# Optimization experiments

Measured on AMD Instinct MI355X. Metric: run time of the kernel, lower is better.

The kernel has to match this reference:

```python
import jax, jax.numpy as jnp
import numpy as np

B, L, D_MODEL = 2, 2048, 256
D_STATE, D_CONV, EXPAND, HEADDIM = 128, 4, 4, 64
D_INNER = EXPAND * D_MODEL            # 1024
NHEADS = D_INNER // HEADDIM           # 16
CONV_DIM = D_INNER + 2 * D_STATE      # 1280
D_IN_PROJ = 2 * D_INNER + 2 * D_STATE + NHEADS  # 2320
CHUNK = 256
GN_EPS = float(np.finfo(np.float32).eps)
RMS_EPS = 1e-5


def _silu(x):
    return x * jax.nn.sigmoid(x)


def _segsum(x):
    # x: (..., T) -> (..., T, T); out[i, j] = sum_{j<k<=i} x[k] for i>=j else -inf
    T = x.shape[-1]
    cs = jnp.cumsum(x, -1)
    d = cs[..., :, None] - cs[..., None, :]
    mask = jnp.tril(jnp.ones((T, T), bool))
    return jnp.where(mask, d, -jnp.inf)


def _ssd(X, A, Bm, Cm):
    # Chunked SSD (Mamba2 ssd_minimal_discrete). X:(b,l,h,p) already dt-scaled,
    # A:(b,l,h) = dt * (-exp(A_log)), Bm/Cm:(b,l,n) with ngroups=1.
    b, l, h, p = X.shape
    c = l // CHUNK
    Xc = X.reshape(b, c, CHUNK, h, p)
    Ac = jnp.transpose(A.reshape(b, c, CHUNK, h), (0, 3, 1, 2))  # (b,h,c,Q)
    Bc = Bm.reshape(b, c, CHUNK, -1)
    Cc = Cm.reshape(b, c, CHUNK, -1)
    A_cs = jnp.cumsum(Ac, -1)                                    # (b,h,c,Q)
    Lmat = jnp.exp(_segsum(Ac))                                  # (b,h,c,Q,Q)
    CB = jnp.einsum('bcln,bcsn->bcls', Cc, Bc)                   # (b,c,Q,Q)
    Y_diag = jnp.einsum('bhcls,bcshp->bclhp', Lmat * CB[:, None], Xc)
    decay_states = jnp.exp(A_cs[..., -1:] - A_cs)                # (b,h,c,Q)
    states = jnp.einsum('bcln,bhcl,bclhp->bchpn', Bc, decay_states, Xc)
    states = jnp.concatenate([jnp.zeros_like(states[:, :1]), states], 1)  # (b,c+1,h,p,n)
    decay_chunk = jnp.exp(_segsum(jnp.pad(A_cs[..., -1], ((0, 0), (0, 0), (1, 0)))))  # (b,h,c+1,c+1)
    new_states = jnp.einsum('bhzc,bchpn->bzhpn', decay_chunk, states)[:, :-1]
    state_decay = jnp.exp(A_cs)                                  # (b,h,c,Q)
    Y_off = jnp.einsum('bcln,bchpn,bhcl->bclhp', Cc, new_states, state_decay)
    return (Y_diag + Y_off).reshape(b, l, h, p)


def _mamba2(u, in_w, conv_w, conv_b, dt_bias, A_log, Dh, norm_w, out_w):
    # u: (b, l, d_model)
    b, l, _ = u.shape
    zxbcdt = u @ in_w.T                                          # (b,l,D_IN_PROJ)
    z = zxbcdt[..., :D_INNER]
    xBC = zxbcdt[..., D_INNER:D_INNER + CONV_DIM]
    dt = jax.nn.softplus(zxbcdt[..., -NHEADS:] + dt_bias)        # (b,l,h)
    # causal depthwise conv over time
    xc = jnp.transpose(xBC, (0, 2, 1))                           # (b,C,l)
    xc = jax.lax.conv_general_dilated(xc, conv_w, (1,), [(D_CONV - 1, 0)],
                                      dimension_numbers=('NCH', 'OIH', 'NCH'),
                                      feature_group_count=CONV_DIM)
    xBC = _silu(jnp.transpose(xc + conv_b[None, :, None], (0, 2, 1)))
    x = xBC[..., :D_INNER].reshape(b, l, NHEADS, HEADDIM)
    Bm = xBC[..., D_INNER:D_INNER + D_STATE]
    Cm = xBC[..., D_INNER + D_STATE:]
    A = dt * (-jnp.exp(A_log))                                   # (b,l,h)
    y = _ssd(dt[..., None] * x, A, Bm, Cm) + x * Dh[None, None, :, None]
    y = y.reshape(b, l, D_INNER) * _silu(z)                      # gated
    y = y * jax.lax.rsqrt(jnp.mean(y * y, -1, keepdims=True) + RMS_EPS) * norm_w
    return y @ out_w.T                                           # (b,l,d_model)


def _resmamba(x, gn_w, gn_b, fp, bp, proj_w, proj_b):
    # GroupNorm(1, C) over (C, L) per sample
    mu = jnp.mean(x, (1, 2), keepdims=True)
    var = jnp.mean((x - mu) ** 2, (1, 2), keepdims=True)
    xn = (x - mu) * jax.lax.rsqrt(var + GN_EPS) * gn_w[None, :, None] + gn_b[None, :, None]
    t = jnp.transpose(xn, (0, 2, 1))                             # (B,L,C)
    fwd = _mamba2(t, *fp)
    bwd = jnp.flip(_mamba2(jnp.flip(t, 1), *bp), 1)
    r = jnp.concatenate([fwd + t, bwd + t], -1)                  # (B,L,2C)
    pr = r @ proj_w.T + proj_b                                   # (B,L,C)
    return x + jnp.transpose(pr, (0, 2, 1))


def setup_inputs():
    key = jax.random.key(0)
    ks = jax.random.split(key, 4)
    s = 0.02
    inp = {
        'x': jax.random.normal(ks[0], (B, D_MODEL, L), jnp.float32),
        'gn_w': jnp.ones((D_MODEL,), jnp.float32),
        'gn_b': jnp.zeros((D_MODEL,), jnp.float32),
        'proj_w': s * jax.random.normal(ks[1], (D_MODEL, 2 * D_MODEL), jnp.float32),
        'proj_b': jnp.zeros((D_MODEL,), jnp.float32),
    }
    for i, p in enumerate(('f', 'b')):
        kk = jax.random.split(ks[2 + i], 5)
        inp[p + '_in_w'] = s * jax.random.normal(kk[0], (D_IN_PROJ, D_MODEL), jnp.float32)
        inp[p + '_conv_w'] = s * jax.random.normal(kk[1], (CONV_DIM, 1, D_CONV), jnp.float32)
        inp[p + '_conv_b'] = jnp.zeros((CONV_DIM,), jnp.float32)
        inp[p + '_dt_bias'] = 0.1 * jax.random.normal(kk[2], (NHEADS,), jnp.float32)
        inp[p + '_A_log'] = jnp.log(jax.random.uniform(kk[3], (NHEADS,), jnp.float32, 1.0, 16.0))
        inp[p + '_D'] = jnp.ones((NHEADS,), jnp.float32)
        inp[p + '_norm_w'] = jnp.ones((D_INNER,), jnp.float32)
        inp[p + '_out_w'] = s * jax.random.normal(kk[4], (D_MODEL, D_INNER), jnp.float32)
    return inp


def reference(x, gn_w, gn_b, proj_w, proj_b,
              f_in_w, f_conv_w, f_conv_b, f_dt_bias, f_A_log, f_D, f_norm_w, f_out_w,
              b_in_w, b_conv_w, b_conv_b, b_dt_bias, b_A_log, b_D, b_norm_w, b_out_w):
    fp = (f_in_w, f_conv_w, f_conv_b, f_dt_bias, f_A_log, f_D, f_norm_w, f_out_w)
    bp = (b_in_w, b_conv_w, b_conv_b, b_dt_bias, b_A_log, b_D, b_norm_w, b_out_w)
    return _resmamba(x, gn_w, gn_b, fp, bp, proj_w, proj_b)
```

## Files before the change

kernel.cpp:

```cpp
#include <hip/hip_runtime.h>
#include <hip/hip_bf16.h>
#include <math.h>

using bf16 = __hip_bfloat16;

#define L_SEQ   2048
#define DMODEL  256
#define DINNER  1024
#define DSTATE  128
#define NH      16
#define HD      64
#define CONVDIM 1280
#define DPROJ   2320
#define NCHK    8
#define CT      256
#define BATCH   2
#define M_TOT   (BATCH*L_SEQ)

#define ACS_N   (BATCH*NH*NCHK*CT)
#define ST_N    ((size_t)BATCH*NCHK*NH*HD*DSTATE)
#define CB_N    ((size_t)BATCH*NCHK*CT*CT)

typedef __bf16 bf16x8_t __attribute__((ext_vector_type(8)));
typedef __bf16 bf16x4_t __attribute__((ext_vector_type(4)));
typedef float  f32x4_t  __attribute__((ext_vector_type(4)));

__device__ __forceinline__ float tof(bf16 v){ return __bfloat162float(v); }
__device__ __forceinline__ bf16  tob(float v){ return __float2bfloat16(v); }
__device__ __forceinline__ float expdec(float a){ return __expf(fminf(a, 0.f)); }

__global__ __launch_bounds__(256) void k_front(
    const float* __restrict__ iw0, const float* __restrict__ iw1, const float* __restrict__ pw,
    bf16* __restrict__ inw_bf, bf16* __restrict__ projw_bf,
    const float* __restrict__ ow0, const float* __restrict__ ow1,
    bf16* __restrict__ owt, bf16* __restrict__ psum,
    const float* __restrict__ x, float2* __restrict__ pbuf){
  __shared__ __bf16 tile[64][65];
  __shared__ float sh[8];
  int bz = blockIdx.x, t = threadIdx.x;
  if (bz < 1160){
    int dir = bz >= 580; int sub = dir ? bz - 580 : bz;
    const float* src = dir ? iw1 : iw0;
    bf16* dst = inw_bf + (size_t)dir*DPROJ*DMODEL;
    int i = (sub*256 + t)*4;
    float4 v = *(const float4*)(src + i);
    dst[i]   = tob(v.x); dst[i+1] = tob(v.y);
    dst[i+2] = tob(v.z); dst[i+3] = tob(v.w);
  } else if (bz < 1288){
    int i = ((bz-1160)*256 + t)*4;
    float4 v = *(const float4*)(pw + i);
    projw_bf[i]   = tob(v.x); projw_bf[i+1] = tob(v.y);
    projw_bf[i+2] = tob(v.z); projw_bf[i+3] = tob(v.w);
  } else if (bz < 1416){
    int sub = bz - 1288;
    int dir = sub >> 6; int tid = sub & 63;
    int k0 = (tid >> 2)*64, j0 = (tid & 3)*64;
    const float* src = dir ? ow1 : ow0;
    bf16* dst = owt + (size_t)dir*DINNER*DMODEL;
    #pragma unroll
    for (int it = 0; it < 2; ++it){
      int idx = t + it*256; int jj = idx >> 3; int k8 = (idx & 7)*8;
      float4 va = *(const float4*)&src[(size_t)(j0+jj)*DINNER + k0 + k8];
      float4 vb = *(const float4*)&src[(size_t)(j0+jj)*DINNER + k0 + k8 + 4];
      tile[k8+0][jj] = (__bf16)va.x; tile[k8+1][jj] = (__bf16)va.y;
      tile[k8+2][jj] = (__bf16)va.z; tile[k8+3][jj] = (__bf16)va.w;
      tile[k8+4][jj] = (__bf16)vb.x; tile[k8+5][jj] = (__bf16)vb.y;
      tile[k8+6][jj] = (__bf16)vb.z; tile[k8+7][jj] = (__bf16)vb.w;
    }
    __syncthreads();
    #pragma unroll
    for (int it = 0; it < 2; ++it){
      int idx = t + it*256; int kr = idx >> 3; int j8 = (idx & 7)*8;
      bf16x8_t o;
      #pragma unroll
      for (int i = 0; i < 8; ++i) o[i] = tile[kr][j8+i];
      *(bf16x8_t*)&dst[(size_t)(k0+kr)*DMODEL + j0 + j8] = o;
    }
  } else if (bz < 1448){
    int i = ((bz - 1416)*256 + t)*8;
    int j = i & 255;
    const float* row = pw + (size_t)(i >> 8)*(2*DMODEL);
    bf16x8_t o;
    #pragma unroll
    for (int c = 0; c < 8; ++c) o[c] = (__bf16)(row[j+c] + row[256+j+c]);
    *(bf16x8_t*)&psum[i] = o;
  } else {
    int sub = bz - 1448;
    int blk = sub & 127, b = sub >> 7;
    const float4* p = (const float4*)(x + (size_t)b*(DMODEL*L_SEQ) + (size_t)blk*4096);
    float s = 0.f, ss = 0.f;
    #pragma unroll
    for (int k = 0; k < 4; ++k){
      float4 v = p[t + k*256];
      s  += v.x + v.y + v.z + v.w;
      ss += v.x*v.x + v.y*v.y + v.z*v.z + v.w*v.w;
    }
    for (int o = 32; o > 0; o >>= 1){ s += __shfl_down(s, o, 64); ss += __shfl_down(ss, o, 64); }
    if ((t & 63) == 0){ sh[(t>>6)*2] = s; sh[(t>>6)*2+1] = ss; }
    __syncthreads();
    if (t == 0){
      s  = sh[0]+sh[2]+sh[4]+sh[6];
      ss = sh[1]+sh[3]+sh[5]+sh[7];
      pbuf[b*128 + blk] = make_float2(s, ss);
    }
  }
}

__global__ __launch_bounds__(256) void k_t(const float* __restrict__ x, const float* __restrict__ gw,
                                           const float* __restrict__ gb, const float2* __restrict__ pbuf,
                                           bf16* __restrict__ t_out){
  __shared__ float tile[64][65];
  __shared__ float sh[4];
  int l0 = blockIdx.x*64, c0 = blockIdx.y*64, b = blockIdx.z;
  int tid = threadIdx.x;
  float s = 0.f, ss = 0.f;
  if (tid < 128){ float2 v = pbuf[b*128 + tid]; s = v.x; ss = v.y; }
  for (int o = 32; o > 0; o >>= 1){ s += __shfl_down(s, o, 64); ss += __shfl_down(ss, o, 64); }
  if (tid < 128 && (tid & 63) == 0){ sh[(tid>>6)*2] = s; sh[(tid>>6)*2+1] = ss; }
  __syncthreads();
  float inv = 1.f/(float)(DMODEL*L_SEQ);
  float s0 = sh[0]+sh[2], ss0 = sh[1]+sh[3];
  float mu = s0*inv, var = ss0*inv - mu*mu;
  float istd = rsqrtf(fmaxf(var, 0.f) + 1.1920929e-07f);

  int lx = tid & 63, cy = tid >> 6;
  for (int cc = cy; cc < 64; cc += 4){
    float v = x[(size_t)b*DMODEL*L_SEQ + (size_t)(c0+cc)*L_SEQ + l0+lx];
    tile[cc][lx] = (v - mu)*istd;
  }
  __syncthreads();
  int cx = tid & 63, ly = tid >> 6;
  float w = gw[c0+cx], bb = gb[c0+cx];
  for (int ll = ly; ll < 64; ll += 4)
    t_out[((size_t)(b*L_SEQ) + l0+ll)*DMODEL + c0+cx] = tob(tile[cx][ll]*w + bb);
}

__global__ __launch_bounds__(256) void gemm_inproj(const bf16* __restrict__ A, const bf16* __restrict__ B,
                                                   bf16* __restrict__ z, bf16* __restrict__ xbc,
                                                   float* __restrict__ dtb,
                                                   const float* __restrict__ db0, const float* __restrict__ db1){
  __shared__ __align__(16) bf16 lds[2][(128+128)*40];
  const int lda = DMODEL, ldb = DMODEL, N = DPROJ;
  int dir = blockIdx.z;
  const bf16* Bd = B + (size_t)dir*(size_t)N*ldb;
  int orig = blockIdx.x;
  int swz = (orig & 7)*76 + (orig >> 3);
  int m0 = (swz & 31)*128;
  int n0 = (swz >> 5)*128;
  int t = threadIdx.x;
  int wave = t >> 6, lane = t & 63;
  int wm = (wave & 1)*64, wn = (wave >> 1)*64;
  int lrow = lane & 15, quad = lane >> 4, lk8 = quad*8;

  int r0 = t >> 2, o0 = (t & 3)*8;
  int r1 = r0 + 64;
  int am0 = m0 + r0, am1 = m0 + r1;
  if (dir){
    am0 = (am0 & ~(L_SEQ-1)) | ((L_SEQ-1) - (am0 & (L_SEQ-1)));
    am1 = (am1 & ~(L_SEQ-1)) | ((L_SEQ-1) - (am1 & (L_SEQ-1)));
  }
  int bn0 = n0 + r0; if (bn0 > N-1) bn0 = N-1;
  int bn1 = n0 + r1; if (bn1 > N-1) bn1 = N-1;
  const bf16* Ap0 = A + (size_t)am0*lda + o0;
  const bf16* Ap1 = A + (size_t)am1*lda + o0;
  const bf16* Bp0 = Bd + (size_t)bn0*ldb + o0;
  const bf16* Bp1 = Bd + (size_t)bn1*ldb + o0;

  f32x4_t acc[4][4];
  #pragma unroll
  for (int i = 0; i < 4; ++i)
    #pragma unroll
    for (int j = 0; j < 4; ++j) acc[i][j] = (f32x4_t){0,0,0,0};

  uint4 ua0 = *(const uint4*)Ap0,      ua1 = *(const uint4*)Ap1;
  uint4 ub0 = *(const uint4*)Bp0,      ub1 = *(const uint4*)Bp1;
  uint4 va0 = *(const uint4*)(Ap0+32), va1 = *(const uint4*)(Ap1+32);
  uint4 vb0 = *(const uint4*)(Bp0+32), vb1 = *(const uint4*)(Bp1+32);

#define STAGE(buf, A0_, A1_, B0_, B1_) \
  *(uint4*)&lds[buf][r0*40 + o0] = A0_; \
  *(uint4*)&lds[buf][r1*40 + o0] = A1_; \
  *(uint4*)&lds[buf][(128 + r0)*40 + o0] = B0_; \
  *(uint4*)&lds[buf][(128 + r1)*40 + o0] = B1_;

#define COMPUTE(buf) { \
  const bf16* cs = lds[buf]; \
  bf16x8_t bfr[4]; \
  _Pragma("unroll") \
  for (int ni = 0; ni < 4; ++ni) bfr[ni] = *(const bf16x8_t*)&cs[(128 + wn + ni*16 + lrow)*40 + lk8]; \
  _Pragma("unroll") \
  for (int mi = 0; mi < 4; ++mi){ \
    bf16x8_t af = *(const bf16x8_t*)&cs[(wm + mi*16 + lrow)*40 + lk8]; \
    _Pragma("unroll") \
    for (int ni = 0; ni < 4; ++ni) \
      acc[mi][ni] = __builtin_amdgcn_mfma_f32_16x16x32_bf16(af, bfr[ni], acc[mi][ni], 0, 0, 0); \
  } }

  STAGE(0, ua0, ua1, ub0, ub1)
  __syncthreads();
  for (int it = 0; it < 8; it += 2){
    if (it + 2 < 8){
      int kk = (it+2) << 5;
      ua0 = *(const uint4*)(Ap0+kk); ua1 = *(const uint4*)(Ap1+kk);
      ub0 = *(const uint4*)(Bp0+kk); ub1 = *(const uint4*)(Bp1+kk);
    }
    COMPUTE(0)
    STAGE(1, va0, va1, vb0, vb1)
    __syncthreads();
    if (it + 3 < 8){
      int kk = (it+3) << 5;
      va0 = *(const uint4*)(Ap0+kk); va1 = *(const uint4*)(Ap1+kk);
      vb0 = *(const uint4*)(Bp0+kk); vb1 = *(const uint4*)(Bp1+kk);
    }
    COMPUTE(1)
    if (it + 2 < 8){
      STAGE(0, ua0, ua1, ub0, ub1)
      __syncthreads();
    }
  }
#undef STAGE
#undef COMPUTE

  if (n0 < DINNER + CONVDIM){
    __syncthreads();
    __bf16* outs = (__bf16*)lds;
    #pragma unroll
    for (int mi = 0; mi < 4; ++mi)
      #pragma unroll
      for (int ni = 0; ni < 4; ++ni)
        #pragma unroll
        for (int r = 0; r < 4; ++r)
          outs[(wm + mi*16 + quad*4 + r)*132 + wn + ni*16 + lrow] = (__bf16)acc[mi][ni][r];
    __syncthreads();
    bf16* dst; int ldd, c0;
    if (n0 < DINNER){ dst = z   + (size_t)dir*M_TOT*DINNER;  ldd = DINNER;  c0 = n0; }
    else            { dst = xbc + (size_t)dir*M_TOT*CONVDIM; ldd = CONVDIM; c0 = n0 - DINNER; }
    #pragma unroll
    for (int itv = 0; itv < 8; ++itv){
      int v = t + itv*256;
      int row = v >> 4, cb = v & 15;
      *(bf16x8_t*)&dst[(size_t)(m0+row)*ldd + c0 + cb*8] =
          *(const bf16x8_t*)&outs[row*132 + cb*8];
    }
  } else {
    const float* db = dir ? db1 : db0;
    float* dtp = dtb + (size_t)dir*((size_t)M_TOT*NH);
    #pragma unroll
    for (int mi = 0; mi < 4; ++mi)
      #pragma unroll
      for (int ni = 0; ni < 4; ++ni)
        #pragma unroll
        for (int r = 0; r < 4; ++r){
          int m = m0 + wm + mi*16 + quad*4 + r;
          int n = n0 + wn + ni*16 + lrow;
          if (n < N){
            int h = n - (DINNER + CONVDIM);
            float xx = acc[mi][ni][r] + db[h];
            dtp[(size_t)m*NH + h] = (xx > 20.f) ? xx : log1pf(expf(xx));
          }
        }
  }
}

__global__ __launch_bounds__(256) void gemm_w(const bf16* __restrict__ P, const bf16* __restrict__ owt,
                                              bf16* __restrict__ W){
  __shared__ __align__(16) bf16 lds[2][(128+64)*40];
  int dir = blockIdx.z;
  int m0 = blockIdx.x*128, n0 = blockIdx.y*64;
  int t = threadIdx.x;
  int wave = t >> 6, lane = t & 63;
  int wm = (wave & 1)*64, wn = (wave >> 1)*32;
  int lrow = lane & 15, quad = lane >> 4, lk8 = quad*8;

  int r0 = t >> 2, o0 = (t & 3)*8;
  int r1 = r0 + 64;
  const bf16* Ap0 = P + (size_t)(m0 + r0)*(2*DMODEL) + dir*DMODEL + o0;
  const bf16* Ap1 = P + (size_t)(m0 + r1)*(2*DMODEL) + dir*DMODEL + o0;
  const bf16* Bp  = owt + (size_t)dir*DINNER*DMODEL + (size_t)(n0 + r0)*DMODEL + o0;

  f32x4_t acc[4][2];
  #pragma unroll
  for (int i = 0; i < 4; ++i){ acc[i][0] = (f32x4_t){0,0,0,0}; acc[i][1] = (f32x4_t){0,0,0,0}; }

  int nit = DMODEL >> 5;
  uint4 a0 = *(const uint4*)Ap0;
  uint4 a1 = *(const uint4*)Ap1;
  uint4 b0 = *(const uint4*)Bp;
  int st = 0;
  *(uint4*)&lds[0][r0*40 + o0] = a0;
  *(uint4*)&lds[0][r1*40 + o0] = a1;
  *(uint4*)&lds[0][(128 + r0)*40 + o0] = b0;
  __syncthreads();
  for (int it = 0; it < nit; ++it){
    bool more = (it+1 < nit);
    if (more){
      int kk = (it+1) << 5;
      a0 = *(const uint4*)(Ap0 + kk);
      a1 = *(const uint4*)(Ap1 + kk);
      b0 = *(const uint4*)(Bp + kk);
    }
    const bf16* cs = lds[st];
    bf16x8_t af[4], bfr[2];
    #pragma unroll
    for (int mi = 0; mi < 4; ++mi) af[mi] = *(const bf16x8_t*)&cs[(wm + mi*16 + lrow)*40 + lk8];
    #pragma unroll
    for (int ni = 0; ni < 2; ++ni) bfr[ni] = *(const bf16x8_t*)&cs[(128 + wn + ni*16 + lrow)*40 + lk8];
    #pragma unroll
    for (int mi = 0; mi < 4; ++mi)
      #pragma unroll
      for (int ni = 0; ni < 2; ++ni)
        acc[mi][ni] = __builtin_amdgcn_mfma_f32_16x16x32_bf16(af[mi], bfr[ni], acc[mi][ni], 0, 0, 0);
    if (more){
      st ^= 1;
      *(uint4*)&lds[st][r0*40 + o0] = a0;
      *(uint4*)&lds[st][r1*40 + o0] = a1;
      *(uint4*)&lds[st][(128 + r0)*40 + o0] = b0;
      __syncthreads();
    }
  }
  bf16* Wd = W + (size_t)dir*DMODEL*DINNER;
  #pragma unroll
  for (int mi = 0; mi < 4; ++mi)
    #pragma unroll
    for (int ni = 0; ni < 2; ++ni)
      #pragma unroll
      for (int r = 0; r < 4; ++r){
        int m = m0 + wm + mi*16 + quad*4 + r;
        int n = n0 + wn + ni*16 + lrow;
        Wd[(size_t)m*DINNER + n] = tob(acc[mi][ni][r]);
      }
}

__global__ __launch_bounds__(256) void gemm_final(const bf16* __restrict__ y, const bf16* __restrict__ tb,
                                                  const bf16* __restrict__ W, const bf16* __restrict__ psum,
                                                  const float* __restrict__ x, const float* __restrict__ pb,
                                                  float* __restrict__ out){
  __shared__ __align__(16) bf16 lds[2][(32+64)*40];
  __shared__ float tile[32][65];
  int orig = blockIdx.x;
  int swz = (orig & 7)*64 + (orig >> 3);
  int mt_ = swz & 127, nt_ = swz >> 7;
  int m0 = mt_*32, n0 = nt_*64;
  int t = threadIdx.x;
  int wave = t >> 6, lane = t & 63;
  int lrow = lane & 15, quad = lane >> 4, lk8 = quad*8;
  int wn = wave*16;

  f32x4_t acc[2];
  acc[0] = (f32x4_t){0,0,0,0}; acc[1] = (f32x4_t){0,0,0,0};

  int rA = t >> 2, oA = (t & 3)*8;

  #pragma unroll
  for (int ph = 0; ph < 3; ++ph){
    const bf16 *Ab, *Bb; int lda, ldb, K, rev;
    if (ph == 0){ Ab = y;                             lda = DINNER; K = DINNER; Bb = W;                             ldb = DINNER; rev = 0; }
    else if (ph == 1){ Ab = y + (size_t)M_TOT*DINNER; lda = DINNER; K = DINNER; Bb = W + (size_t)DMODEL*DINNER;     ldb = DINNER; rev = 1; }
    else { Ab = tb; lda = DMODEL; K = DMODEL; Bb = psum; ldb = DMODEL; rev = 0; }

    int am = m0 + rA;
    if (rev) am = (am & ~(L_SEQ-1)) | ((L_SEQ-1) - (am & (L_SEQ-1)));
    const bf16* Ap = Ab + (size_t)am*lda + oA;
    const bf16* Bp = Bb + (size_t)(n0 + rA)*ldb + oA;

    int nit = K >> 5;
    uint4 a0, b0;
    if (t < 128) a0 = *(const uint4*)Ap;
    b0 = *(const uint4*)Bp;
    __syncthreads();
    int st = 0;
    if (t < 128) *(uint4*)&lds[0][rA*40 + oA] = a0;
    *(uint4*)&lds[0][(32 + rA)*40 + oA] = b0;
    __syncthreads();
    for (int it = 0; it < nit; ++it){
      bool more = (it+1 < nit);
      if (more){
        int kk = (it+1) << 5;
        if (t < 128) a0 = *(const uint4*)(Ap + kk);
        b0 = *(const uint4*)(Bp + kk);
      }
      const bf16* cs = lds[st];
      bf16x8_t bq = *(const bf16x8_t*)&cs[(32 + wn + lrow)*40 + lk8];
      #pragma unroll
      for (int mt = 0; mt < 2; ++mt){
        bf16x8_t af = *(const bf16x8_t*)&cs[(mt*16 + lrow)*40 + lk8];
        acc[mt] = __builtin_amdgcn_mfma_f32_16x16x32_bf16(af, bq, acc[mt], 0, 0, 0);
      }
      if (more){
        st ^= 1;
        if (t < 128) *(uint4*)&lds[st][rA*40 + oA] = a0;
        *(uint4*)&lds[st][(32 + rA)*40 + oA] = b0;
        __syncthreads();
      }
    }
  }

  #pragma unroll
  for (int mt = 0; mt < 2; ++mt)
    #pragma unroll
    for (int r = 0; r < 4; ++r)
      tile[mt*16 + quad*4 + r][wn + lrow] = acc[mt][r];
  __syncthreads();
  int b = m0 >> 11, l0 = m0 & (L_SEQ-1);
  int tx = t & 31, ny = t >> 5;
  for (int nn = ny; nn < 64; nn += 8){
    int n = n0 + nn;
    size_t xi = (size_t)b*DMODEL*L_SEQ + (size_t)n*L_SEQ + l0 + tx;
    out[xi] = tile[tx][nn] + pb[n] + x[xi];
  }
}

__global__ __launch_bounds__(256) void k_conv(const bf16* __restrict__ xraw, const float* __restrict__ cw0,
                                              const float* __restrict__ cb0, const float* __restrict__ cw1,
                                              const float* __restrict__ cb1, bf16* __restrict__ xconv){
  int t = threadIdx.x;
  int tx = t & 31, ty = t >> 5;
  int ch0 = blockIdx.x*256 + tx*8;
  int z = blockIdx.z; int b = z & 1, dir = z >> 1;
  int lbase = blockIdx.y*32 + ty*4;
  const float* cw = dir ? cw1 : cw0;
  const float* cb = dir ? cb1 : cb0;
  const bf16* xr = xraw  + (size_t)dir*((size_t)M_TOT*CONVDIM) + (size_t)(b*L_SEQ)*CONVDIM + ch0;
  bf16* xcv      = xconv + (size_t)dir*((size_t)M_TOT*CONVDIM) + (size_t)(b*L_SEQ)*CONVDIM + ch0;

  float wk[4][8];
  #pragma unroll
  for (int c = 0; c < 8; ++c){
    float4 w = *(const float4*)&cw[(ch0+c)*4];
    wk[0][c] = w.x; wk[1][c] = w.y; wk[2][c] = w.z; wk[3][c] = w.w;
  }
  float bias[8];
  {
    float4 b0v = *(const float4*)&cb[ch0];
    float4 b1v = *(const float4*)&cb[ch0+4];
    bias[0]=b0v.x; bias[1]=b0v.y; bias[2]=b0v.z; bias[3]=b0v.w;
    bias[4]=b1v.x; bias[5]=b1v.y; bias[6]=b1v.z; bias[7]=b1v.w;
  }

  bf16x8_t zero;
  #pragma unroll
  for (int c = 0; c < 8; ++c) zero[c] = (__bf16)0.f;

  bf16x8_t win[4];
  #pragma unroll
  for (int k = 0; k < 3; ++k){
    int ls = lbase - 3 + k;
    win[k] = (ls >= 0) ? *(const bf16x8_t*)&xr[(size_t)ls*CONVDIM] : zero;
  }
  #pragma unroll
  for (int i = 0; i < 4; ++i){
    int l = lbase + i;
    win[3] = *(const bf16x8_t*)&xr[(size_t)l*CONVDIM];
    bf16x8_t outv;
    #pragma unroll
    for (int c = 0; c < 8; ++c){
      float a = bias[c] + (float)win[0][c]*wk[0][c] + (float)win[1][c]*wk[1][c]
                        + (float)win[2][c]*wk[2][c] + (float)win[3][c]*wk[3][c];
      outv[c] = (__bf16)(a / (1.f + __expf(-a)));
    }
    *(bf16x8_t*)&xcv[(size_t)l*CONVDIM] = outv;
    win[0] = win[1]; win[1] = win[2]; win[2] = win[3];
  }
}

__global__ __launch_bounds__(256) void k_states(const bf16* __restrict__ xconv, const float* __restrict__ dt,
                                                const float* __restrict__ Al0, const float* __restrict__ Al1,
                                                float* __restrict__ A_cs, float* __restrict__ states){
  int id0 = blockIdx.x;
  int dir = id0 >> 8; int id = id0 & 255;
  int h = id & 15; int bc = id >> 4; int ch = bc & 7; int b = bc >> 3;
  int t = threadIdx.x;
  __shared__ float s_acs[CT];
  __shared__ float w_s[CT];
  __shared__ __align__(16) __bf16 Xt[64*72];
  __shared__ __align__(16) __bf16 Bt[128*72];
  const bf16* xc = xconv + (size_t)dir*((size_t)M_TOT*CONVDIM);
  const float* dtp = dt + (size_t)dir*((size_t)M_TOT*NH);
  const float* Alog = dir ? Al1 : Al0;
  size_t rowbase = (size_t)(b*L_SEQ) + ch*CT;

  float dtv = dtp[(rowbase + t)*NH + h];
  s_acs[t] = -expf(Alog[h]) * dtv;
  __syncthreads();
  for (int off = 1; off < 256; off <<= 1){
    float v = (t >= off) ? s_acs[t-off] : 0.f;
    __syncthreads();
    s_acs[t] += v;
    __syncthreads();
  }
  A_cs[(size_t)dir*ACS_N + (size_t)((b*NH+h)*NCHK + ch)*CT + t] = s_acs[t];
  float alast = s_acs[CT-1];
  w_s[t] = dtv * __expf(fminf(alast - s_acs[t], 0.f));
  __syncthreads();

  int wave = t >> 6, lane = t & 63, lrow = lane & 15, quad = lane >> 4;
  f32x4_t acc[8];
  #pragma unroll
  for (int i = 0; i < 8; ++i) acc[i] = (f32x4_t){0.f,0.f,0.f,0.f};

  for (int kt = 0; kt < 4; ++kt){
    int l0 = kt*64;
    #pragma unroll
    for (int it = 0; it < 2; ++it){
      int idx = t + it*256; int l = idx >> 3; int p0 = (idx & 7)*8;
      bf16x8_t v = *(const bf16x8_t*)&xc[(rowbase + l0 + l)*CONVDIM + h*HD + p0];
      float w = w_s[l0 + l];
      int col = (((l>>3) ^ ((p0>>3)&7))<<3) | (l&7);
      #pragma unroll
      for (int j = 0; j < 8; ++j) Xt[(p0+j)*72 + col] = (__bf16)((float)v[j]*w);
    }
    #pragma unroll
    for (int it = 0; it < 4; ++it){
      int idx = t + it*256; int l = idx >> 4; int n0 = (idx & 15)*8;
      bf16x8_t v = *(const bf16x8_t*)&xc[(rowbase + l0 + l)*CONVDIM + DINNER + n0];
      int col = (((l>>3) ^ ((n0>>3)&7))<<3) | (l&7);
      #pragma unroll
      for (int j = 0; j < 8; ++j) Bt[(n0+j)*72 + col] = v[j];
    }
    __syncthreads();
    int arow = wave*16 + lrow;
    #pragma unroll
    for (int ks = 0; ks < 2; ++ks){
      int kg = ks*4 + quad;
      bf16x8_t af = *(const bf16x8_t*)&Xt[arow*72 + ((kg ^ ((arow>>3)&7))<<3)];
      #pragma unroll
      for (int nt = 0; nt < 8; ++nt){
        int brow = nt*16 + lrow;
        bf16x8_t bq = *(const bf16x8_t*)&Bt[brow*72 + ((kg ^ ((brow>>3)&7))<<3)];
        acc[nt] = __builtin_amdgcn_mfma_f32_16x16x32_bf16(af, bq, acc[nt], 0, 0, 0);
      }
    }
    __syncthreads();
  }
  float* so = states + (size_t)dir*ST_N + (size_t)id*HD*DSTATE;
  int m = wave*16 + quad*4;
  #pragma unroll
  for (int nt = 0; nt < 8; ++nt)
    #pragma unroll
    for (int r = 0; r < 4; ++r)
      so[(size_t)(m+r)*DSTATE + nt*16 + lrow] = acc[nt][r];
}

__global__ __launch_bounds__(256) void k_recur(float* __restrict__ states, const float* __restrict__ A_cs){
  int blk = blockIdx.x;
  int bh2 = blk >> 5;
  int e = (blk & 31)*256 + threadIdx.x;
  int dir = bh2 >> 5; int bh = bh2 & 31;
  int h = bh & 15, b = bh >> 4;
  const float* ac = A_cs + (size_t)dir*ACS_N;
  float* st = states + (size_t)dir*ST_N;
  float s = 0.f;
  #pragma unroll
  for (int ch = 0; ch < NCHK; ++ch){
    float dec = expdec(ac[((size_t)(bh*NCHK+ch))*CT + CT-1]);
    size_t off = (size_t)(((b*NCHK+ch)*NH)+h)*HD*DSTATE + e;
    float cur = st[off];
    st[off] = s;
    s = s*dec + cur;
  }
}

__global__ __launch_bounds__(256) void k_cb(const bf16* __restrict__ xconv, float* __restrict__ CB){
  int zz = blockIdx.z;
  int dir = zz >> 4; int b = (zz >> 3) & 1; int ch = zz & 7;
  int m0 = blockIdx.x*64, n0 = blockIdx.y*64;
  if (n0 > m0) return;
  const bf16* base = xconv + (size_t)dir*((size_t)M_TOT*CONVDIM) + (size_t)(b*L_SEQ + ch*CT)*CONVDIM;
  const bf16* Crow = base + DINNER + DSTATE;
  const bf16* Brow = base + DINNER;
  __shared__ __align__(16) __bf16 As[64*136];
  __shared__ __align__(16) __bf16 Bs[64*136];
  int t = threadIdx.x;
  int r = t >> 2, o0 = (t & 3)*32;
  #pragma unroll
  for (int j = 0; j < 4; ++j){
    *(bf16x8_t*)&As[r*136 + o0 + j*8] = *(const bf16x8_t*)&Crow[(size_t)(m0+r)*CONVDIM + o0 + j*8];
    *(bf16x8_t*)&Bs[r*136 + o0 + j*8] = *(const bf16x8_t*)&Brow[(size_t)(n0+r)*CONVDIM + o0 + j*8];
  }
  __syncthreads();
  int wave = t >> 6, lane = t & 63, lrow = lane & 15, quad = lane >> 4;
  int wm = wave*16;
  f32x4_t acc[4];
  #pragma unroll
  for (int i = 0; i < 4; ++i) acc[i] = (f32x4_t){0.f,0.f,0.f,0.f};
  #pragma unroll
  for (int ks = 0; ks < 4; ++ks){
    bf16x8_t af = *(const bf16x8_t*)&As[(wm+lrow)*136 + ks*32 + quad*8];
    #pragma unroll
    for (int nt = 0; nt < 4; ++nt){
      bf16x8_t bq = *(const bf16x8_t*)&Bs[(nt*16+lrow)*136 + ks*32 + quad*8];
      acc[nt] = __builtin_amdgcn_mfma_f32_16x16x32_bf16(af, bq, acc[nt], 0, 0, 0);
    }
  }
  float* outp = CB + (size_t)dir*CB_N + (size_t)(b*NCHK+ch)*CT*CT;
  #pragma unroll
  for (int nt = 0; nt < 4; ++nt)
    #pragma unroll
    for (int r2 = 0; r2 < 4; ++r2)
      outp[(size_t)(m0+wm+quad*4+r2)*CT + n0+nt*16+lrow] = acc[nt][r2];
}

__global__ __launch_bounds__(512) void k_y_mfma(const bf16* __restrict__ xconv, const float* __restrict__ dt,
                                                const float* __restrict__ A_cs, const float* __restrict__ CB,
                                                const float* __restrict__ ns, bf16* __restrict__ y){
  int id0 = blockIdx.x;
  int dir = id0 >> 8; int id = id0 & 255;
  int h = id & 15; int bc = id >> 4; int ch = bc & 7; int b = bc >> 3;
  int t = threadIdx.x;
  int lane = t & 63;
  int lrow = lane & 15, quad = lane >> 4;

  __shared__ __align__(16) bf16 Xs[64*264];
  __shared__ __align__(16) bf16 NSs[64*136];
  __shared__ float acs_s[CT];

  const bf16* xc = xconv + (size_t)dir*((size_t)M_TOT*CONVDIM);
  const float* dtp = dt + (size_t)dir*((size_t)M_TOT*NH);
  const float* acs = A_cs + (size_t)dir*ACS_N + (size_t)((b*NH+h)*NCHK + ch)*CT;
  const float* cbz = CB + (size_t)dir*CB_N + (size_t)(b*NCHK+ch)*CT*CT;
  const float* nsp = ns + (size_t)dir*ST_N + (size_t)(((b*NCHK+ch)*NH)+h)*HD*DSTATE;
  bf16* yp = y + (size_t)dir*((size_t)M_TOT*DINNER);
  size_t rowbase = (size_t)(b*L_SEQ + ch*CT);
  if (t < CT) acs_s[t] = acs[t];

  #pragma unroll
  for (int it = 0; it < 4; ++it){
    int idx = t + it*512;
    int s = idx >> 3, p0 = (idx & 7)*8;
    float dtv = dtp[(rowbase + s)*NH + h];
    bf16x8_t v = *(const bf16x8_t*)&xc[(rowbase + s)*CONVDIM + h*HD + p0];
    int col = ((((s>>3) ^ ((p0>>3)&7)))<<3) | (s&7);
    #pragma unroll
    for (int j = 0; j < 8; ++j)
      Xs[(p0+j)*264 + col] = tob((float)v[j] * dtv);
  }
  for (int it = 0; it < 4; ++it){
    int idx = t + it*512;
    int n4 = (idx & 31)*4, p = idx >> 5;
    float4 v = *(const float4*)(nsp + p*DSTATE + n4);
    bf16* w = &NSs[p*136 + n4];
    w[0] = tob(v.x); w[1] = tob(v.y); w[2] = tob(v.z); w[3] = tob(v.w);
  }
  __syncthreads();

  int wave = t >> 6;
  int row0 = wave*32;
  float al0 = acs_s[row0 + lrow];
  float al1 = acs_s[row0 + 16 + lrow];
  float acs_r0 = acs_s[row0];

  f32x4_t acc[2][4];
  #pragma unroll
  for (int i = 0; i < 2; ++i)
    #pragma unroll
    for (int j = 0; j < 4; ++j) acc[i][j] = (f32x4_t){0.f,0.f,0.f,0.f};

  int nst = (row0 + 32) >> 5;
  for (int st = 0; st < nst; ++st){
    int s0 = st*32;
    if (s0 + 31 < row0 && (acs_r0 - acs_s[s0+31]) < -30.f) continue;
    int sg = (s0 >> 3) + quad;
    bf16x8_t bq[4];
    #pragma unroll
    for (int nt = 0; nt < 4; ++nt){
      int brow = nt*16 + lrow;
      bq[nt] = *(const bf16x8_t*)&Xs[brow*264 + ((sg ^ ((brow>>3)&7))<<3)];
    }
    bf16x8_t af[2];
    #pragma unroll
    for (int mt = 0; mt < 2; ++mt){
      int l = row0 + mt*16 + lrow;
      float al = mt ? al1 : al0;
      const float* cbrow = cbz + (size_t)l*CT + s0 + quad*8;
      float4 c0 = *(const float4*)cbrow;
      float4 c1 = *(const float4*)(cbrow + 4);
      float cv[8] = {c0.x,c0.y,c0.z,c0.w,c1.x,c1.y,c1.z,c1.w};
      union { bf16x8_t v; __bf16 e[8]; } wa;
      #pragma unroll
      for (int j = 0; j < 8; ++j){
        int s = s0 + quad*8 + j;
        float w = (s <= l) ? __expf(fminf(al - acs_s[s], 0.f)) * cv[j] : 0.f;
        wa.e[j] = (__bf16)w;
      }
      af[mt] = wa.v;
    }
    #pragma unroll
    for (int mt = 0; mt < 2; ++mt)
      #pragma unroll
      for (int nt = 0; nt < 4; ++nt)
        acc[mt][nt] = __builtin_amdgcn_mfma_f32_16x16x32_bf16(af[mt], bq[nt], acc[mt][nt], 0, 0, 0);
  }

  float el0 = __expf(fminf(al0, 0.f));
  float el1 = __expf(fminf(al1, 0.f));
  #pragma unroll
  for (int kt = 0; kt < 4; ++kt){
    int n0 = kt*32;
    bf16x8_t bq[4];
    #pragma unroll
    for (int nt = 0; nt < 4; ++nt)
      bq[nt] = *(const bf16x8_t*)&NSs[(nt*16+lrow)*136 + n0 + quad*8];
    bf16x8_t af[2];
    #pragma unroll
    for (int mt = 0; mt < 2; ++mt){
      int l = row0 + mt*16 + lrow;
      float el = mt ? el1 : el0;
      union { bf16x8_t v; __bf16 e[8]; } cu;
      cu.v = *(const bf16x8_t*)&xc[(rowbase + l)*CONVDIM + DINNER + DSTATE + n0 + quad*8];
      union { bf16x8_t v; __bf16 e[8]; } wa;
      #pragma unroll
      for (int j = 0; j < 8; ++j) wa.e[j] = (__bf16)((float)cu.e[j] * el);
      af[mt] = wa.v;
    }
    #pragma unroll
    for (int mt = 0; mt < 2; ++mt)
      #pragma unroll
      for (int nt = 0; nt < 4; ++nt)
        acc[mt][nt] = __builtin_amdgcn_mfma_f32_16x16x32_bf16(af[mt], bq[nt], acc[mt][nt], 0, 0, 0);
  }

  #pragma unroll
  for (int mt = 0; mt < 2; ++mt)
    #pragma unroll
    for (int nt = 0; nt < 4; ++nt)
      #pragma unroll
      for (int rr = 0; rr < 4; ++rr){
        int l = row0 + mt*16 + quad*4 + rr;
        int p = nt*16 + lrow;
        yp[(rowbase + l)*DINNER + h*HD + p] = tob(acc[mt][nt][rr]);
      }
}

__global__ __launch_bounds__(256) void k_gaterms(const bf16* __restrict__ z, const float* __restrict__ nw0,
                                                 const float* __restrict__ nw1, const bf16* __restrict__ xconv,
                                                 const float* __restrict__ Dh0, const float* __restrict__ Dh1,
                                                 bf16* __restrict__ y){
  int m0 = blockIdx.x;
  int dir = m0 >> 12; int m = m0 & (M_TOT-1);
  int t = threadIdx.x;
  const float* nw = dir ? nw1 : nw0;
  const float* Dh = dir ? Dh1 : Dh0;
  int j0 = t*4;
  const bf16* zp = z + (size_t)dir*((size_t)M_TOT*DINNER) + (size_t)m*DINNER;
  const bf16* xc = xconv + (size_t)dir*((size_t)M_TOT*CONVDIM) + (size_t)m*CONVDIM;
  bf16* yp = y + (size_t)dir*((size_t)M_TOT*DINNER) + (size_t)m*DINNER;

  bf16x4_t zv = *(const bf16x4_t*)&zp[j0];
  bf16x4_t yv = *(const bf16x4_t*)&yp[j0];
  bf16x4_t xv = *(const bf16x4_t*)&xc[j0];
  float Dv = Dh[j0 >> 6];
  float v[4]; float ss = 0.f;
  #pragma unroll
  for (int c = 0; c < 4; ++c){
    float zf = (float)zv[c];
    float raw = (float)yv[c] + Dv*(float)xv[c];
    float g = raw * (zf / (1.f + __expf(-zf)));
    v[c] = g; ss += g*g;
  }
  for (int o = 32; o > 0; o >>= 1) ss += __shfl_down(ss, o, 64);
  __shared__ float sh[4];
  if ((t & 63) == 0) sh[t>>6] = ss;
  __syncthreads();
  ss = sh[0]+sh[1]+sh[2]+sh[3];
  float scale = rsqrtf(ss*(1.f/DINNER) + 1e-5f);
  float4 nwv = *(const float4*)&nw[j0];
  float nws[4] = {nwv.x, nwv.y, nwv.z, nwv.w};
  bf16x4_t o;
  #pragma unroll
  for (int c = 0; c < 4; ++c) o[c] = (__bf16)(v[c]*scale*nws[c]);
  *(bf16x4_t*)&yp[j0] = o;
}

extern "C" void kernel_launch(void* const* d_in, const int* in_sizes, int n_in,
                              void* d_out, int out_size, void* d_ws, size_t ws_size,
                              hipStream_t stream){
  (void)in_sizes; (void)n_in; (void)out_size; (void)ws_size;
  const float* x      = (const float*)d_in[0];
  const float* gn_w   = (const float*)d_in[1];
  const float* gn_b   = (const float*)d_in[2];
  const float* proj_w = (const float*)d_in[3];
  const float* proj_b = (const float*)d_in[4];
  float* out = (float*)d_out;

  char* wp = (char*)d_ws;
  auto alloc = [&](size_t bytes){ void* r = (void*)wp; wp += (bytes + 255) & ~(size_t)255; return r; };
  bf16*  t_buf  = (bf16*) alloc((size_t)M_TOT*DMODEL*2);
  bf16*  z_buf  = (bf16*) alloc((size_t)2*M_TOT*DINNER*2);
  bf16*  xraw   = (bf16*) alloc((size_t)2*M_TOT*CONVDIM*2);
  bf16*  xconv  = (bf16*) alloc((size_t)2*M_TOT*CONVDIM*2);
  float* dt_buf = (float*)alloc((size_t)2*M_TOT*NH*4);
  float* acs    = (float*)alloc((size_t)2*ACS_N*4);
  float* states = (float*)alloc((size_t)2*ST_N*4);
  float* cb     = (float*)alloc((size_t)2*CB_N*4);
  float2* pbuf  = (float2*)alloc(BATCH*128*sizeof(float2));
  bf16*  inw_bf   = (bf16*)alloc((size_t)2*DPROJ*DMODEL*2);
  bf16*  projw_bf = (bf16*)alloc((size_t)DMODEL*2*DMODEL*2);
  bf16*  owt      = (bf16*)alloc((size_t)2*DINNER*DMODEL*2);
  bf16*  wfb      = (bf16*)alloc((size_t)2*DMODEL*DINNER*2);
  bf16*  psum     = (bf16*)alloc((size_t)DMODEL*DMODEL*2);
  bf16*  y_buf    = xraw;

  k_front<<<1704, 256, 0, stream>>>(
      (const float*)d_in[5], (const float*)d_in[13], proj_w,
      inw_bf, projw_bf,
      (const float*)d_in[12], (const float*)d_in[20], owt, psum,
      x, pbuf);

  gemm_w<<<dim3(2, 16, 2), 256, 0, stream>>>(projw_bf, owt, wfb);

  k_t<<<dim3(32,4,2), 256, 0, stream>>>(x, gn_w, gn_b, pbuf, t_buf);

  gemm_inproj<<<dim3(608, 1, 2), 256, 0, stream>>>(
      t_buf, inw_bf, z_buf, xraw, dt_buf,
      (const float*)d_in[8], (const float*)d_in[16]);

  k_conv<<<dim3(5, L_SEQ/32, 2*BATCH), 256, 0, stream>>>(
      xraw, (const float*)d_in[6], (const float*)d_in[7],
            (const float*)d_in[14], (const float*)d_in[15], xconv);
  k_states<<<2*BATCH*NCHK*NH, 256, 0, stream>>>(
      xconv, dt_buf, (const float*)d_in[9], (const float*)d_in[17], acs, states);
  k_recur<<<2*BATCH*NH*32, 256, 0, stream>>>(states, acs);
  k_cb<<<dim3(4,4,2*BATCH*NCHK), 256, 0, stream>>>(xconv, cb);
  k_y_mfma<<<2*BATCH*NCHK*NH, 512, 0, stream>>>(xconv, dt_buf, acs, cb, states, y_buf);
  k_gaterms<<<2*M_TOT, 256, 0, stream>>>(
      z_buf, (const float*)d_in[11], (const float*)d_in[19], xconv,
      (const float*)d_in[10], (const float*)d_in[18], y_buf);

  gemm_final<<<512, 256, 0, stream>>>(y_buf, t_buf, wfb, psum, x, proj_b, out);
}
```

Baseline: 227.5 us.

## Store CB and chunk states in bf16; widen gemm_final K-tile to 64

k_recur now writes the propagated chunk states to a separate bf16 buffer, and k_cb stages its output through LDS to write bf16 CB with vectorized stores. k_y_mfma reads both as bf16, which halves the bytes it loads and removes its per-element float-to-bf16 conversion. gemm_final moves from a 32-wide K step to a 64-wide one, with all threads loading and an unrolled double-buffered prologue, so it needs fewer barriers per K. Rounding CB to bf16 before the decay weighting adds a little extra error.

```diff
diff --git a/kernel.cpp b/kernel.cpp
--- a/kernel.cpp
+++ b/kernel.cpp
@@ -335,7 +335,7 @@
                                                   const bf16* __restrict__ W, const bf16* __restrict__ psum,
                                                   const float* __restrict__ x, const float* __restrict__ pb,
                                                   float* __restrict__ out){
-  __shared__ __align__(16) bf16 lds[2][(32+64)*40];
+  __shared__ __align__(16) bf16 lds[2][(32+64)*72];
   __shared__ float tile[32][65];
   int orig = blockIdx.x;
   int swz = (orig & 7)*64 + (orig >> 3);
@@ -349,7 +349,9 @@
   f32x4_t acc[2];
   acc[0] = (f32x4_t){0,0,0,0}; acc[1] = (f32x4_t){0,0,0,0};
 
-  int rA = t >> 2, oA = (t & 3)*8;
+  int rowA = t >> 3, oA = (t & 7)*8;
+  int rowB0 = t >> 3, oB0 = (t & 7)*8;
+  int rowB1 = (t + 256) >> 3, oB1 = (t & 7)*8;
 
   #pragma unroll
   for (int ph = 0; ph < 3; ++ph){
@@ -358,41 +360,60 @@
     else if (ph == 1){ Ab = y + (size_t)M_TOT*DINNER; lda = DINNER; K = DINNER; Bb = W + (size_t)DMODEL*DINNER;     ldb = DINNER; rev = 1; }
     else { Ab = tb; lda = DMODEL; K = DMODEL; Bb = psum; ldb = DMODEL; rev = 0; }
 
-    int am = m0 + rA;
+    int am = m0 + rowA;
     if (rev) am = (am & ~(L_SEQ-1)) | ((L_SEQ-1) - (am & (L_SEQ-1)));
-    const bf16* Ap = Ab + (size_t)am*lda + oA;
-    const bf16* Bp = Bb + (size_t)(n0 + rA)*ldb + oA;
-
-    int nit = K >> 5;
-    uint4 a0, b0;
-    if (t < 128) a0 = *(const uint4*)Ap;
-    b0 = *(const uint4*)Bp;
-    __syncthreads();
-    int st = 0;
-    if (t < 128) *(uint4*)&lds[0][rA*40 + oA] = a0;
-    *(uint4*)&lds[0][(32 + rA)*40 + oA] = b0;
-    __syncthreads();
-    for (int it = 0; it < nit; ++it){
-      bool more = (it+1 < nit);
-      if (more){
-        int kk = (it+1) << 5;
-        if (t < 128) a0 = *(const uint4*)(Ap + kk);
-        b0 = *(const uint4*)(Bp + kk);
+    const bf16* Ap  = Ab + (size_t)am*lda + oA;
+    const bf16* Bp0 = Bb + (size_t)(n0 + rowB0)*ldb + oB0;
+    const bf16* Bp1 = Bb + (size_t)(n0 + rowB1)*ldb + oB1;
+
+    int nit = K >> 6;
+    uint4 au  = *(const uint4*)Ap;
+    uint4 bu0 = *(const uint4*)Bp0;
+    uint4 bu1 = *(const uint4*)Bp1;
+    uint4 av  = *(const uint4*)(Ap + 64);
+    uint4 bv0 = *(const uint4*)(Bp0 + 64);
+    uint4 bv1 = *(const uint4*)(Bp1 + 64);
+
+#define FSTAGE(buf, A_, B0_, B1_) \
+    *(uint4*)&lds[buf][rowA*72 + oA] = A_; \
+    *(uint4*)&lds[buf][(32 + rowB0)*72 + oB0] = B0_; \
+    *(uint4*)&lds[buf][(32 + rowB1)*72 + oB1] = B1_;
+
+#define FCOMP(buf) { \
+    const bf16* cs = lds[buf]; \
+    _Pragma("unroll") \
+    for (int ks = 0; ks < 2; ++ks){ \
+      bf16x8_t bq = *(const bf16x8_t*)&cs[(32 + wn + lrow)*72 + ks*32 + lk8]; \
+      _Pragma("unroll") \
+      for (int mt = 0; mt < 2; ++mt){ \
+        bf16x8_t af = *(const bf16x8_t*)&cs[(mt*16 + lrow)*72 + ks*32 + lk8]; \
+        acc[mt] = __builtin_amdgcn_mfma_f32_16x16x32_bf16(af, bq, acc[mt], 0, 0, 0); \
+      } \
+    } }
+
+    __syncthreads();
+    FSTAGE(0, au, bu0, bu1)
+    __syncthreads();
+    for (int it = 0; it < nit; it += 2){
+      if (it + 2 < nit){
+        int kk = (it+2) << 6;
+        au = *(const uint4*)(Ap+kk); bu0 = *(const uint4*)(Bp0+kk); bu1 = *(const uint4*)(Bp1+kk);
       }
-      const bf16* cs = lds[st];
-      bf16x8_t bq = *(const bf16x8_t*)&cs[(32 + wn + lrow)*40 + lk8];
-      #pragma unroll
-      for (int mt = 0; mt < 2; ++mt){
-        bf16x8_t af = *(const bf16x8_t*)&cs[(mt*16 + lrow)*40 + lk8];
-        acc[mt] = __builtin_amdgcn_mfma_f32_16x16x32_bf16(af, bq, acc[mt], 0, 0, 0);
+      FCOMP(0)
+      FSTAGE(1, av, bv0, bv1)
+      __syncthreads();
+      if (it + 3 < nit){
+        int kk = (it+3) << 6;
+        av = *(const uint4*)(Ap+kk); bv0 = *(const uint4*)(Bp0+kk); bv1 = *(const uint4*)(Bp1+kk);
       }
-      if (more){
-        st ^= 1;
-        if (t < 128) *(uint4*)&lds[st][rA*40 + oA] = a0;
-        *(uint4*)&lds[st][(32 + rA)*40 + oA] = b0;
+      FCOMP(1)
+      if (it + 2 < nit){
+        FSTAGE(0, au, bu0, bu1)
         __syncthreads();
       }
     }
+#undef FSTAGE
+#undef FCOMP
   }
 
   #pragma unroll
@@ -541,26 +562,28 @@
       so[(size_t)(m+r)*DSTATE + nt*16 + lrow] = acc[nt][r];
 }
 
-__global__ __launch_bounds__(256) void k_recur(float* __restrict__ states, const float* __restrict__ A_cs){
+__global__ __launch_bounds__(256) void k_recur(const float* __restrict__ states, bf16* __restrict__ nsb,
+                                               const float* __restrict__ A_cs){
   int blk = blockIdx.x;
   int bh2 = blk >> 5;
   int e = (blk & 31)*256 + threadIdx.x;
   int dir = bh2 >> 5; int bh = bh2 & 31;
   int h = bh & 15, b = bh >> 4;
   const float* ac = A_cs + (size_t)dir*ACS_N;
-  float* st = states + (size_t)dir*ST_N;
+  const float* st = states + (size_t)dir*ST_N;
+  bf16* nb = nsb + (size_t)dir*ST_N;
   float s = 0.f;
   #pragma unroll
   for (int ch = 0; ch < NCHK; ++ch){
     float dec = expdec(ac[((size_t)(bh*NCHK+ch))*CT + CT-1]);
     size_t off = (size_t)(((b*NCHK+ch)*NH)+h)*HD*DSTATE + e;
     float cur = st[off];
-    st[off] = s;
+    nb[off] = tob(s);
     s = s*dec + cur;
   }
 }
 
-__global__ __launch_bounds__(256) void k_cb(const bf16* __restrict__ xconv, float* __restrict__ CB){
+__global__ __launch_bounds__(256) void k_cb(const bf16* __restrict__ xconv, bf16* __restrict__ CB){
   int zz = blockIdx.z;
   int dir = zz >> 4; int b = (zz >> 3) & 1; int ch = zz & 7;
   int m0 = blockIdx.x*64, n0 = blockIdx.y*64;
@@ -592,17 +615,25 @@
       acc[nt] = __builtin_amdgcn_mfma_f32_16x16x32_bf16(af, bq, acc[nt], 0, 0, 0);
     }
   }
-  float* outp = CB + (size_t)dir*CB_N + (size_t)(b*NCHK+ch)*CT*CT;
+  __syncthreads();
   #pragma unroll
   for (int nt = 0; nt < 4; ++nt)
     #pragma unroll
     for (int r2 = 0; r2 < 4; ++r2)
-      outp[(size_t)(m0+wm+quad*4+r2)*CT + n0+nt*16+lrow] = acc[nt][r2];
+      As[(wm + quad*4 + r2)*72 + nt*16 + lrow] = (__bf16)acc[nt][r2];
+  __syncthreads();
+  bf16* outp = CB + (size_t)dir*CB_N + (size_t)(b*NCHK+ch)*CT*CT;
+  #pragma unroll
+  for (int p = 0; p < 2; ++p){
+    int idx = t + p*256;
+    int row = idx >> 3, c8 = (idx & 7)*8;
+    *(bf16x8_t*)&outp[(size_t)(m0+row)*CT + n0 + c8] = *(const bf16x8_t*)&As[row*72 + c8];
+  }
 }
 
 __global__ __launch_bounds__(512) void k_y_mfma(const bf16* __restrict__ xconv, const float* __restrict__ dt,
-                                                const float* __restrict__ A_cs, const float* __restrict__ CB,
-                                                const float* __restrict__ ns, bf16* __restrict__ y){
+                                                const float* __restrict__ A_cs, const bf16* __restrict__ CB,
+                                                const bf16* __restrict__ ns, bf16* __restrict__ y){
   int id0 = blockIdx.x;
   int dir = id0 >> 8; int id = id0 & 255;
   int h = id & 15; int bc = id >> 4; int ch = bc & 7; int b = bc >> 3;
@@ -617,8 +648,8 @@
   const bf16* xc = xconv + (size_t)dir*((size_t)M_TOT*CONVDIM);
   const float* dtp = dt + (size_t)dir*((size_t)M_TOT*NH);
   const float* acs = A_cs + (size_t)dir*ACS_N + (size_t)((b*NH+h)*NCHK + ch)*CT;
-  const float* cbz = CB + (size_t)dir*CB_N + (size_t)(b*NCHK+ch)*CT*CT;
-  const float* nsp = ns + (size_t)dir*ST_N + (size_t)(((b*NCHK+ch)*NH)+h)*HD*DSTATE;
+  const bf16* cbz = CB + (size_t)dir*CB_N + (size_t)(b*NCHK+ch)*CT*CT;
+  const bf16* nsp = ns + (size_t)dir*ST_N + (size_t)(((b*NCHK+ch)*NH)+h)*HD*DSTATE;
   bf16* yp = y + (size_t)dir*((size_t)M_TOT*DINNER);
   size_t rowbase = (size_t)(b*L_SEQ + ch*CT);
   if (t < CT) acs_s[t] = acs[t];
@@ -634,12 +665,11 @@
     for (int j = 0; j < 8; ++j)
       Xs[(p0+j)*264 + col] = tob((float)v[j] * dtv);
   }
-  for (int it = 0; it < 4; ++it){
+  #pragma unroll
+  for (int it = 0; it < 2; ++it){
     int idx = t + it*512;
-    int n4 = (idx & 31)*4, p = idx >> 5;
-    float4 v = *(const float4*)(nsp + p*DSTATE + n4);
-    bf16* w = &NSs[p*136 + n4];
-    w[0] = tob(v.x); w[1] = tob(v.y); w[2] = tob(v.z); w[3] = tob(v.w);
+    int p = idx >> 4, n8 = (idx & 15)*8;
+    *(bf16x8_t*)&NSs[p*136 + n8] = *(const bf16x8_t*)&nsp[(size_t)p*DSTATE + n8];
   }
   __syncthreads();
 
@@ -671,15 +701,12 @@
     for (int mt = 0; mt < 2; ++mt){
       int l = row0 + mt*16 + lrow;
       float al = mt ? al1 : al0;
-      const float* cbrow = cbz + (size_t)l*CT + s0 + quad*8;
-      float4 c0 = *(const float4*)cbrow;
-      float4 c1 = *(const float4*)(cbrow + 4);
-      float cv[8] = {c0.x,c0.y,c0.z,c0.w,c1.x,c1.y,c1.z,c1.w};
+      bf16x8_t cvv = *(const bf16x8_t*)&cbz[(size_t)l*CT + s0 + quad*8];
       union { bf16x8_t v; __bf16 e[8]; } wa;
       #pragma unroll
       for (int j = 0; j < 8; ++j){
         int s = s0 + quad*8 + j;
-        float w = (s <= l) ? __expf(fminf(al - acs_s[s], 0.f)) * cv[j] : 0.f;
+        float w = (s <= l) ? __expf(fminf(al - acs_s[s], 0.f)) * (float)cvv[j] : 0.f;
         wa.e[j] = (__bf16)w;
       }
       af[mt] = wa.v;
@@ -791,7 +818,8 @@
   float* dt_buf = (float*)alloc((size_t)2*M_TOT*NH*4);
   float* acs    = (float*)alloc((size_t)2*ACS_N*4);
   float* states = (float*)alloc((size_t)2*ST_N*4);
-  float* cb     = (float*)alloc((size_t)2*CB_N*4);
+  bf16*  nsb    = (bf16*) alloc((size_t)2*ST_N*2);
+  bf16*  cb     = (bf16*) alloc((size_t)2*CB_N*2);
   float2* pbuf  = (float2*)alloc(BATCH*128*sizeof(float2));
   bf16*  inw_bf   = (bf16*)alloc((size_t)2*DPROJ*DMODEL*2);
   bf16*  projw_bf = (bf16*)alloc((size_t)DMODEL*2*DMODEL*2);
@@ -819,9 +847,9 @@
             (const float*)d_in[14], (const float*)d_in[15], xconv);
   k_states<<<2*BATCH*NCHK*NH, 256, 0, stream>>>(
       xconv, dt_buf, (const float*)d_in[9], (const float*)d_in[17], acs, states);
-  k_recur<<<2*BATCH*NH*32, 256, 0, stream>>>(states, acs);
+  k_recur<<<2*BATCH*NH*32, 256, 0, stream>>>(states, nsb, acs);
   k_cb<<<dim3(4,4,2*BATCH*NCHK), 256, 0, stream>>>(xconv, cb);
-  k_y_mfma<<<2*BATCH*NCHK*NH, 512, 0, stream>>>(xconv, dt_buf, acs, cb, states, y_buf);
+  k_y_mfma<<<2*BATCH*NCHK*NH, 512, 0, stream>>>(xconv, dt_buf, acs, cb, nsb, y_buf);
   k_gaterms<<<2*M_TOT, 256, 0, stream>>>(
       z_buf, (const float*)d_in[11], (const float*)d_in[19], xconv,
       (const float*)d_in[10], (const float*)d_in[18], y_buf);
```

After: 221.4 us. -2.7%, faster.
